# Performance work log

Hardware: AMD Instinct MI355X
Metric: run time of the kernel (lower is better)

The kernel has to match this reference:

```python
import jax, jax.numpy as jnp
import numpy as np

LN_EPS = 1e-5


def setup_inputs() -> dict:
    key = jax.random.key(0)
    ks = jax.random.split(key, 6)
    T, B, D, O, G = 32, 4096, 128, 128, 9
    x = jax.random.normal(ks[0], (T, B, D), dtype=jnp.float32)
    sequence_mask = jnp.ones((T, B, 1), dtype=bool)
    # freq: arange(1,G+1)/(G+1)  (norm_freq=True, is_first=False)
    freq = (jnp.arange(1, G + 1, dtype=jnp.float32) / (G + 1)).reshape(1, 1, 1, G)
    # phase buffer: grid_phase + input_phase + small perturbations
    grid_phase = jnp.linspace(0.0, np.pi, G).reshape(1, 1, 1, G)
    input_phase = jnp.linspace(0.0, np.pi, D).reshape(1, 1, D, 1)
    gp_pert = jax.random.uniform(ks[1], (1, 1, 1, G)) / G * 0.1
    ip_pert = jax.random.uniform(ks[2], (1, 1, D, 1)) / D * 0.1
    phase = (grid_phase + input_phase + gp_pert + ip_pert).astype(jnp.float32)
    # amplitudes: uniform(-1,1)/O / grid_norm_factor  -> (O, D, G)
    grid_norm = (jnp.arange(G, dtype=jnp.float32) + 1.0).reshape(1, 1, G)
    amplitudes = (jax.random.uniform(ks[3], (O, D, 1), minval=-1.0, maxval=1.0) / O) / grid_norm
    bias = jnp.ones((1, O), dtype=jnp.float32) / O
    ln_weight = jnp.ones((D,), dtype=jnp.float32)
    ln_bias = jnp.zeros((D,), dtype=jnp.float32)
    return {"x": x, "sequence_mask": sequence_mask, "freq": freq, "phase": phase,
            "amplitudes": amplitudes, "bias": bias, "ln_weight": ln_weight, "ln_bias": ln_bias}


def reference(x, sequence_mask, freq, phase, amplitudes, bias, ln_weight, ln_bias):
    T, B, D = x.shape
    O, _, G = amplitudes.shape
    # LayerNorm over feature dim
    mu = jnp.mean(x, axis=-1, keepdims=True)
    var = jnp.mean(jnp.square(x - mu), axis=-1, keepdims=True)
    xn = (x - mu) * jax.lax.rsqrt(var + LN_EPS) * ln_weight + ln_bias
    xf = xn.reshape(T * B, D)
    # sine basis expansion: (N, D, G)
    s = jnp.sin(xf[:, :, None] * freq.reshape(1, 1, G) + phase.reshape(1, D, G))
    # contraction to output dim: (N, O)
    y = jnp.einsum('nkg,okg->no', s, amplitudes) + bias
    y = y.reshape(T, B, O)
    return y * sequence_mask.astype(y.dtype)
```

## Files before the change

kernel.cpp:

```cpp
#include <hip/hip_runtime.h>
#include <hip/hip_bf16.h>

typedef __attribute__((ext_vector_type(8))) short short8;
typedef __attribute__((ext_vector_type(16))) float f32x16;

#define D_DIM 128
#define G_DIM 9
#define O_DIM 128
#define K_DIM (D_DIM * G_DIM)
#define ROWS 128
#define PAD 8
#define LDK (D_DIM + PAD)

__device__ __forceinline__ float fast_sin(float x) {
  return __builtin_amdgcn_sinf(x * 0.15915494309189535f);
}

__device__ __forceinline__ short f2bf(float f) {
  unsigned u = __float_as_uint(f);
  unsigned r = (u + 0x7FFFu + ((u >> 16) & 1u)) >> 16;
  return (short)r;
}

__global__ void sinekan_prep(const float* __restrict__ amp,
                             const float* __restrict__ phase,
                             short* __restrict__ Bp,
                             float* __restrict__ pt,
                             int total) {
  int i = blockIdx.x * blockDim.x + threadIdx.x;
  if (i < total) {
    int o = i / K_DIM;
    int rem = i - o * K_DIM;
    int g = rem >> 7;
    int d = rem & 127;
    Bp[i] = f2bf(amp[(o * D_DIM + d) * G_DIM + g]);
  }
  if (i < K_DIM) {
    int g = i >> 7, d = i & 127;
    pt[i] = phase[d * G_DIM + g];
  }
}

__global__ __launch_bounds__(256, 2)
void sinekan_fused(const float* __restrict__ x,
                   const int* __restrict__ mask,
                   const float* __restrict__ freq,
                   const float* __restrict__ bias,
                   const float* __restrict__ lnw,
                   const float* __restrict__ lnb,
                   const short* __restrict__ Bp,
                   const float* __restrict__ pt,
                   float* __restrict__ out) {
  __shared__ short s_lds[ROWS * LDK];
  __shared__ short b_lds[O_DIM * LDK];
  __shared__ float mu_s[ROWS], rs_s[ROWS], mk_s[ROWS];
  __shared__ float w_s[D_DIM], bb_s[D_DIM];

  const int tid = threadIdx.x;
  const int row0 = blockIdx.x * ROWS;

  if (tid < D_DIM) { w_s[tid] = lnw[tid]; bb_s[tid] = lnb[tid]; }
  if (tid < ROWS)  { mk_s[tid] = mask[row0 + tid] ? 1.0f : 0.0f; }

  {
    int r = tid >> 1, h = tid & 1;
    const float4* xp = (const float4*)(x + (size_t)(row0 + r) * D_DIM + h * 64);
    float s = 0.f, sq = 0.f;
#pragma unroll
    for (int i = 0; i < 16; ++i) {
      float4 v = xp[i];
      s  += v.x + v.y + v.z + v.w;
      sq += v.x * v.x + v.y * v.y + v.z * v.z + v.w * v.w;
    }
    s  += __shfl_xor(s, 1, 64);
    sq += __shfl_xor(sq, 1, 64);
    if (h == 0) {
      float m = s * (1.0f / 128.0f);
      float var = sq * (1.0f / 128.0f) - m * m;
      mu_s[r] = m;
      rs_s[r] = rsqrtf(var + 1e-5f);
    }
  }
  __syncthreads();

  const int dcol = (tid & 15) * 8;
  float xc[8][8];
#pragma unroll
  for (int sw = 0; sw < 8; ++sw) {
    int r = sw * 16 + (tid >> 4);
    const float4* xp = (const float4*)(x + (size_t)(row0 + r) * D_DIM + dcol);
    float4 v0 = xp[0], v1 = xp[1];
    float m = mu_s[r], rst = rs_s[r];
    float xv[8] = {v0.x, v0.y, v0.z, v0.w, v1.x, v1.y, v1.z, v1.w};
#pragma unroll
    for (int j = 0; j < 8; ++j)
      xc[sw][j] = (xv[j] - m) * rst * w_s[dcol + j] + bb_s[dcol + j];
  }

  const int lane = tid & 63;
  const int wv   = tid >> 6;
  const int rbase = (wv >> 1) * 64;
  const int cbase = (wv & 1) * 64;
  const int lr = lane & 31;
  const int hi = lane >> 5;

  f32x16 acc[2][2] = {};

  for (int g = 0; g < G_DIM; ++g) {
    const float fg = freq[g];

#pragma unroll
    for (int sw = 0; sw < 8; ++sw) {
      int r = sw * 16 + (tid >> 4);
      const float4* pp = (const float4*)(pt + g * D_DIM + dcol);
      float4 p0 = pp[0], p1 = pp[1];
      float ph[8] = {p0.x, p0.y, p0.z, p0.w, p1.x, p1.y, p1.z, p1.w};
      short8 pk;
#pragma unroll
      for (int j = 0; j < 8; ++j)
        pk[j] = f2bf(fast_sin(fmaf(xc[sw][j], fg, ph[j])));
      *(short8*)&s_lds[r * LDK + dcol] = pk;
    }

#pragma unroll
    for (int sw = 0; sw < 8; ++sw) {
      int idx = sw * 256 + tid;
      int o  = idx >> 4;
      int un = idx & 15;
      short8 bv = *(const short8*)&Bp[o * K_DIM + g * D_DIM + un * 8];
      *(short8*)&b_lds[o * LDK + un * 8] = bv;
    }
    __syncthreads();

#pragma unroll
    for (int kk = 0; kk < 8; ++kk) {
      int ko = kk * 16 + hi * 8;
      short8 a0 = *(const short8*)&s_lds[(rbase + lr)      * LDK + ko];
      short8 a1 = *(const short8*)&s_lds[(rbase + 32 + lr) * LDK + ko];
      short8 b0 = *(const short8*)&b_lds[(cbase + lr)      * LDK + ko];
      short8 b1 = *(const short8*)&b_lds[(cbase + 32 + lr) * LDK + ko];
      acc[0][0] = __builtin_amdgcn_mfma_f32_32x32x16_bf16(a0, b0, acc[0][0], 0, 0, 0);
      acc[0][1] = __builtin_amdgcn_mfma_f32_32x32x16_bf16(a0, b1, acc[0][1], 0, 0, 0);
      acc[1][0] = __builtin_amdgcn_mfma_f32_32x32x16_bf16(a1, b0, acc[1][0], 0, 0, 0);
      acc[1][1] = __builtin_amdgcn_mfma_f32_32x32x16_bf16(a1, b1, acc[1][1], 0, 0, 0);
    }
    __syncthreads();
  }

#pragma unroll
  for (int mt = 0; mt < 2; ++mt) {
#pragma unroll
    for (int nt = 0; nt < 2; ++nt) {
      int col = cbase + nt * 32 + lr;
      float bv = bias[col];
#pragma unroll
      for (int reg = 0; reg < 16; ++reg) {
        int rit  = (reg & 3) + 8 * (reg >> 2) + 4 * hi;
        int rloc = rbase + mt * 32 + rit;
        float y = (acc[mt][nt][reg] + bv) * mk_s[rloc];
        out[(size_t)(row0 + rloc) * O_DIM + col] = y;
      }
    }
  }
}

extern "C" void kernel_launch(void* const* d_in, const int* in_sizes, int n_in,
                              void* d_out, int out_size, void* d_ws, size_t ws_size,
                              hipStream_t stream) {
  const float* x    = (const float*)d_in[0];
  const int* mk     = (const int*)d_in[1];
  const float* freq = (const float*)d_in[2];
  const float* phase= (const float*)d_in[3];
  const float* amp  = (const float*)d_in[4];
  const float* bias = (const float*)d_in[5];
  const float* lnw  = (const float*)d_in[6];
  const float* lnb  = (const float*)d_in[7];
  float* out = (float*)d_out;

  int N = in_sizes[0] / D_DIM;
  short* Bp = (short*)d_ws;
  float* pt = (float*)((char*)d_ws + (size_t)O_DIM * K_DIM * sizeof(short));

  int total = O_DIM * K_DIM;
  sinekan_prep<<<(total + 255) / 256, 256, 0, stream>>>(amp, phase, Bp, pt, total);
  sinekan_fused<<<N / ROWS, 256, 0, stream>>>(x, mk, freq, bias, lnw, lnb, Bp, pt, out);
}
```

Before: 174.6 us.

## Double-buffer B tiles via direct-to-LDS loads and compute sine in registers

Restructures the fused kernel so each wave owns 64 rows against all 128 outputs, with 256 rows per block. Sine features are computed directly into MFMA A-fragments in registers instead of going through shared memory. The amplitude tiles are laid out g-major and XOR-swizzled, then loaded with global_load_lds into a double buffer so the next g's tile is prefetched during compute. This removes one barrier per g. Phase and freq are prescaled by 1/2π, and the normalized input is held as bf16 in registers. That adds extra rounding of the input before the sine argument, and 8 accumulators raise register pressure.

```diff
diff --git a/kernel.cpp b/kernel.cpp
--- a/kernel.cpp
+++ b/kernel.cpp
@@ -3,18 +3,15 @@
 
 typedef __attribute__((ext_vector_type(8))) short short8;
 typedef __attribute__((ext_vector_type(16))) float f32x16;
+typedef __attribute__((ext_vector_type(4))) unsigned uint4v;
+typedef unsigned int u32;
 
 #define D_DIM 128
 #define G_DIM 9
 #define O_DIM 128
-#define K_DIM (D_DIM * G_DIM)
-#define ROWS 128
-#define PAD 8
-#define LDK (D_DIM + PAD)
-
-__device__ __forceinline__ float fast_sin(float x) {
-  return __builtin_amdgcn_sinf(x * 0.15915494309189535f);
-}
+#define K_DIM 1152
+#define BROWS 256
+#define INV2PI 0.15915494309189535f
 
 __device__ __forceinline__ short f2bf(float f) {
   unsigned u = __float_as_uint(f);
@@ -22,143 +19,176 @@
   return (short)r;
 }
 
+__device__ __forceinline__ float bf2f(short s) {
+  return __uint_as_float(((unsigned)(unsigned short)s) << 16);
+}
+
+__device__ __forceinline__ unsigned pk2bf(float a, float b) {
+  __hip_bfloat162 h = __float22bfloat162_rn(float2{a, b});
+  return *reinterpret_cast<unsigned*>(&h);
+}
+
 __global__ void sinekan_prep(const float* __restrict__ amp,
                              const float* __restrict__ phase,
+                             const float* __restrict__ freq,
                              short* __restrict__ Bp,
-                             float* __restrict__ pt,
-                             int total) {
+                             float* __restrict__ pt2,
+                             float* __restrict__ fq2) {
   int i = blockIdx.x * blockDim.x + threadIdx.x;
-  if (i < total) {
-    int o = i / K_DIM;
-    int rem = i - o * K_DIM;
-    int g = rem >> 7;
-    int d = rem & 127;
-    Bp[i] = f2bf(amp[(o * D_DIM + d) * G_DIM + g]);
+  if (i < G_DIM * O_DIM * D_DIM) {
+    int g = i >> 14, rem = i & 16383, o = rem >> 7, d = rem & 127;
+    Bp[(g << 14) + (o << 7) + (d ^ ((o & 7) << 3))] = f2bf(amp[(o * D_DIM + d) * G_DIM + g]);
   }
   if (i < K_DIM) {
     int g = i >> 7, d = i & 127;
-    pt[i] = phase[d * G_DIM + g];
+    pt2[i] = phase[d * G_DIM + g] * INV2PI;
+  }
+  if (i < G_DIM) fq2[i] = freq[i] * INV2PI;
+}
+
+__device__ __forceinline__ void stage_b(const short* __restrict__ Bp, short* dst_lds,
+                                        int g, int tid) {
+  const char* src = (const char*)Bp + ((size_t)g << 15) + tid * 16;
+  char* dst = (char*)dst_lds + (tid >> 6) * 1024;
+#pragma unroll
+  for (int c = 0; c < 8; ++c) {
+    __builtin_amdgcn_global_load_lds(
+        (const __attribute__((address_space(1))) u32*)(src + c * 4096),
+        (__attribute__((address_space(3))) u32*)(dst + c * 4096), 16, 0, 0);
   }
 }
 
 __global__ __launch_bounds__(256, 2)
 void sinekan_fused(const float* __restrict__ x,
                    const int* __restrict__ mask,
-                   const float* __restrict__ freq,
                    const float* __restrict__ bias,
                    const float* __restrict__ lnw,
                    const float* __restrict__ lnb,
                    const short* __restrict__ Bp,
-                   const float* __restrict__ pt,
+                   const float* __restrict__ pt2,
+                   const float* __restrict__ fq2,
                    float* __restrict__ out) {
-  __shared__ short s_lds[ROWS * LDK];
-  __shared__ short b_lds[O_DIM * LDK];
-  __shared__ float mu_s[ROWS], rs_s[ROWS], mk_s[ROWS];
+  __shared__ short b_lds[2][O_DIM * D_DIM];
+  __shared__ float pt_lds[G_DIM * D_DIM];
+  __shared__ float mu_s[BROWS], rs_s[BROWS], mk_s[BROWS];
   __shared__ float w_s[D_DIM], bb_s[D_DIM];
 
   const int tid = threadIdx.x;
-  const int row0 = blockIdx.x * ROWS;
+  const int row0 = blockIdx.x * BROWS;
+  const int wv = tid >> 6, lane = tid & 63, lr = lane & 31, hi = lane >> 5;
+
+  stage_b(Bp, b_lds[0], 0, tid);
 
   if (tid < D_DIM) { w_s[tid] = lnw[tid]; bb_s[tid] = lnb[tid]; }
-  if (tid < ROWS)  { mk_s[tid] = mask[row0 + tid] ? 1.0f : 0.0f; }
+  mk_s[tid] = mask[row0 + tid] ? 1.0f : 0.0f;
+  for (int i = tid; i < G_DIM * D_DIM; i += 256) pt_lds[i] = pt2[i];
 
   {
-    int r = tid >> 1, h = tid & 1;
-    const float4* xp = (const float4*)(x + (size_t)(row0 + r) * D_DIM + h * 64);
-    float s = 0.f, sq = 0.f;
-#pragma unroll
-    for (int i = 0; i < 16; ++i) {
-      float4 v = xp[i];
-      s  += v.x + v.y + v.z + v.w;
-      sq += v.x * v.x + v.y * v.y + v.z * v.z + v.w * v.w;
-    }
-    s  += __shfl_xor(s, 1, 64);
-    sq += __shfl_xor(sq, 1, 64);
-    if (h == 0) {
-      float m = s * (1.0f / 128.0f);
-      float var = sq * (1.0f / 128.0f) - m * m;
-      mu_s[r] = m;
-      rs_s[r] = rsqrtf(var + 1e-5f);
+    int rloc = tid >> 4, ch = tid & 15;
+#pragma unroll 1
+    for (int it = 0; it < 16; ++it) {
+      int r = it * 16 + rloc;
+      const float4* xp = (const float4*)(x + (size_t)(row0 + r) * D_DIM + ch * 8);
+      float4 a = xp[0], b = xp[1];
+      float s  = a.x + a.y + a.z + a.w + b.x + b.y + b.z + b.w;
+      float sq = a.x*a.x + a.y*a.y + a.z*a.z + a.w*a.w
+               + b.x*b.x + b.y*b.y + b.z*b.z + b.w*b.w;
+#pragma unroll
+      for (int off = 1; off < 16; off <<= 1) {
+        s  += __shfl_xor(s, off, 64);
+        sq += __shfl_xor(sq, off, 64);
+      }
+      if (ch == 0) {
+        float m = s * (1.0f / 128.0f);
+        mu_s[r] = m;
+        rs_s[r] = rsqrtf(sq * (1.0f / 128.0f) - m * m + 1e-5f);
+      }
     }
   }
   __syncthreads();
 
-  const int dcol = (tid & 15) * 8;
-  float xc[8][8];
-#pragma unroll
-  for (int sw = 0; sw < 8; ++sw) {
-    int r = sw * 16 + (tid >> 4);
-    const float4* xp = (const float4*)(x + (size_t)(row0 + r) * D_DIM + dcol);
-    float4 v0 = xp[0], v1 = xp[1];
-    float m = mu_s[r], rst = rs_s[r];
-    float xv[8] = {v0.x, v0.y, v0.z, v0.w, v1.x, v1.y, v1.z, v1.w};
-#pragma unroll
-    for (int j = 0; j < 8; ++j)
-      xc[sw][j] = (xv[j] - m) * rst * w_s[dcol + j] + bb_s[dcol + j];
-  }
-
-  const int lane = tid & 63;
-  const int wv   = tid >> 6;
-  const int rbase = (wv >> 1) * 64;
-  const int cbase = (wv & 1) * 64;
-  const int lr = lane & 31;
-  const int hi = lane >> 5;
-
-  f32x16 acc[2][2] = {};
-
+  short8 xnc[2][8];
+#pragma unroll
+  for (int m = 0; m < 2; ++m) {
+    const int rl = wv * 64 + m * 32 + lr;
+    const float mu = mu_s[rl], rs = rs_s[rl];
+    const float* xr = x + (size_t)(row0 + rl) * D_DIM;
+#pragma unroll
+    for (int kk = 0; kk < 8; ++kk) {
+      const int d0 = kk * 16 + hi * 8;
+      float4 xa = *(const float4*)(xr + d0);
+      float4 xb = *(const float4*)(xr + d0 + 4);
+      float xv[8] = {xa.x, xa.y, xa.z, xa.w, xb.x, xb.y, xb.z, xb.w};
+      uint4v pk;
+#pragma unroll
+      for (int jj = 0; jj < 4; ++jj) {
+        float e0 = (xv[2*jj]   - mu) * rs * w_s[d0 + 2*jj]   + bb_s[d0 + 2*jj];
+        float e1 = (xv[2*jj+1] - mu) * rs * w_s[d0 + 2*jj+1] + bb_s[d0 + 2*jj+1];
+        pk[jj] = pk2bf(e0, e1);
+      }
+      xnc[m][kk] = __builtin_bit_cast(short8, pk);
+    }
+  }
+  __syncthreads();
+
+  const int swz = (lr & 7) << 4;
+  f32x16 acc[2][4] = {};
+
+#pragma unroll 1
   for (int g = 0; g < G_DIM; ++g) {
-    const float fg = freq[g];
-
-#pragma unroll
-    for (int sw = 0; sw < 8; ++sw) {
-      int r = sw * 16 + (tid >> 4);
-      const float4* pp = (const float4*)(pt + g * D_DIM + dcol);
-      float4 p0 = pp[0], p1 = pp[1];
-      float ph[8] = {p0.x, p0.y, p0.z, p0.w, p1.x, p1.y, p1.z, p1.w};
-      short8 pk;
-#pragma unroll
-      for (int j = 0; j < 8; ++j)
-        pk[j] = f2bf(fast_sin(fmaf(xc[sw][j], fg, ph[j])));
-      *(short8*)&s_lds[r * LDK + dcol] = pk;
-    }
-
-#pragma unroll
-    for (int sw = 0; sw < 8; ++sw) {
-      int idx = sw * 256 + tid;
-      int o  = idx >> 4;
-      int un = idx & 15;
-      short8 bv = *(const short8*)&Bp[o * K_DIM + g * D_DIM + un * 8];
-      *(short8*)&b_lds[o * LDK + un * 8] = bv;
+    if (g + 1 < G_DIM) stage_b(Bp, b_lds[(g + 1) & 1], g + 1, tid);
+    const float fg2v = fq2[g];
+    const short* bl = b_lds[g & 1];
+    const float* ptg = pt_lds + (g << 7);
+
+#pragma unroll
+    for (int kk = 0; kk < 8; ++kk) {
+      const int d0 = kk * 16 + hi * 8;
+      float4 p0 = *(const float4*)(ptg + d0);
+      float4 p1 = *(const float4*)(ptg + d0 + 4);
+      const float ph[8] = {p0.x, p0.y, p0.z, p0.w, p1.x, p1.y, p1.z, p1.w};
+
+      short8 af[2];
+#pragma unroll
+      for (int m = 0; m < 2; ++m) {
+        uint4v pk;
+#pragma unroll
+        for (int jj = 0; jj < 4; ++jj) {
+          float a0 = fmaf(bf2f(xnc[m][kk][2*jj]),     fg2v, ph[2*jj]);
+          float a1 = fmaf(bf2f(xnc[m][kk][2*jj + 1]), fg2v, ph[2*jj + 1]);
+          float s0 = __builtin_amdgcn_sinf(a0);
+          float s1 = __builtin_amdgcn_sinf(a1);
+          pk[jj] = pk2bf(s0, s1);
+        }
+        af[m] = __builtin_bit_cast(short8, pk);
+      }
+
+      const int kx = (kk * 32 + hi * 16) ^ swz;
+      short8 bf[4];
+#pragma unroll
+      for (int n = 0; n < 4; ++n)
+        bf[n] = *(const short8*)((const char*)bl + (((n * 32 + lr) << 8) + kx));
+
+#pragma unroll
+      for (int m = 0; m < 2; ++m)
+#pragma unroll
+        for (int n = 0; n < 4; ++n)
+          acc[m][n] = __builtin_amdgcn_mfma_f32_32x32x16_bf16(af[m], bf[n], acc[m][n], 0, 0, 0);
     }
     __syncthreads();
-
-#pragma unroll
-    for (int kk = 0; kk < 8; ++kk) {
-      int ko = kk * 16 + hi * 8;
-      short8 a0 = *(const short8*)&s_lds[(rbase + lr)      * LDK + ko];
-      short8 a1 = *(const short8*)&s_lds[(rbase + 32 + lr) * LDK + ko];
-      short8 b0 = *(const short8*)&b_lds[(cbase + lr)      * LDK + ko];
-      short8 b1 = *(const short8*)&b_lds[(cbase + 32 + lr) * LDK + ko];
-      acc[0][0] = __builtin_amdgcn_mfma_f32_32x32x16_bf16(a0, b0, acc[0][0], 0, 0, 0);
-      acc[0][1] = __builtin_amdgcn_mfma_f32_32x32x16_bf16(a0, b1, acc[0][1], 0, 0, 0);
-      acc[1][0] = __builtin_amdgcn_mfma_f32_32x32x16_bf16(a1, b0, acc[1][0], 0, 0, 0);
-      acc[1][1] = __builtin_amdgcn_mfma_f32_32x32x16_bf16(a1, b1, acc[1][1], 0, 0, 0);
-    }
-    __syncthreads();
-  }
-
-#pragma unroll
-  for (int mt = 0; mt < 2; ++mt) {
-#pragma unroll
-    for (int nt = 0; nt < 2; ++nt) {
-      int col = cbase + nt * 32 + lr;
+  }
+
+#pragma unroll
+  for (int m = 0; m < 2; ++m) {
+#pragma unroll
+    for (int n = 0; n < 4; ++n) {
+      int col = n * 32 + lr;
       float bv = bias[col];
 #pragma unroll
       for (int reg = 0; reg < 16; ++reg) {
         int rit  = (reg & 3) + 8 * (reg >> 2) + 4 * hi;
-        int rloc = rbase + mt * 32 + rit;
-        float y = (acc[mt][nt][reg] + bv) * mk_s[rloc];
-        out[(size_t)(row0 + rloc) * O_DIM + col] = y;
+        int rloc = wv * 64 + m * 32 + rit;
+        out[(size_t)(row0 + rloc) * O_DIM + col] = (acc[m][n][reg] + bv) * mk_s[rloc];
       }
     }
   }
@@ -179,9 +209,10 @@
 
   int N = in_sizes[0] / D_DIM;
   short* Bp = (short*)d_ws;
-  float* pt = (float*)((char*)d_ws + (size_t)O_DIM * K_DIM * sizeof(short));
-
-  int total = O_DIM * K_DIM;
-  sinekan_prep<<<(total + 255) / 256, 256, 0, stream>>>(amp, phase, Bp, pt, total);
-  sinekan_fused<<<N / ROWS, 256, 0, stream>>>(x, mk, freq, bias, lnw, lnb, Bp, pt, out);
-}
+  float* pt2 = (float*)((char*)d_ws + (size_t)G_DIM * O_DIM * D_DIM * sizeof(short));
+  float* fq2 = pt2 + G_DIM * D_DIM;
+
+  int total = G_DIM * O_DIM * D_DIM;
+  sinekan_prep<<<(total + 255) / 256, 256, 0, stream>>>(amp, phase, freq, Bp, pt2, fq2);
+  sinekan_fused<<<N / BROWS, 256, 0, stream>>>(x, mk, bias, lnw, lnb, Bp, pt2, fq2, out);
+}
```

Result: slower. 199.7 us (+14.3%).
